# Kernel optimization log

Hardware: AMD Instinct MI355X
Metric: run time of the kernel (lower is better)

The kernel has to match this reference:

```python
import jax, jax.numpy as jnp
import numpy as np

B, S, H, D, R = 16, 2048, 1024, 64, 2048  # batch, seq_len, hidden, inner_dim, num_relations


def setup_inputs() -> dict:
    key = jax.random.key(0)
    k1, k2, k3, k4 = jax.random.split(key, 4)
    last_hidden_state = jax.random.normal(k1, (B, S, H), dtype=jnp.float32)
    W = jax.random.normal(k2, (H, 2 * D), dtype=jnp.float32) * (H ** -0.5)
    b = jnp.zeros((2 * D,), dtype=jnp.float32)
    position_ids = jnp.tile(jnp.arange(S, dtype=jnp.int32), (B, 1))
    relations_idx = jax.random.randint(k3, (B, R, 4), 0, S, dtype=jnp.int32)
    labels_mask = (jax.random.uniform(k4, (B, R)) > 0.1).astype(jnp.float32)
    return {
        'last_hidden_state': last_hidden_state,
        'W': W,
        'b': b,
        'position_ids': position_ids,
        'relations_idx': relations_idx,
        'labels_mask': labels_mask,
    }


def reference(last_hidden_state, W, b, position_ids, relations_idx, labels_mask):
    # linear projection -> split into q/k halves
    outputs = last_hidden_state @ W + b            # [B,S,2D]
    qw, kw = outputs[..., :D], outputs[..., D:]    # each [B,S,D]

    # RoPE (interleaved sin/cos layout matching torch stack+reshape)
    inv_freq = jnp.power(10000.0, -2.0 * jnp.arange(D // 2, dtype=jnp.float32) / D)
    ang = position_ids[..., None].astype(jnp.float32) * inv_freq  # [B,S,D/2]
    sin_pos = jnp.repeat(jnp.sin(ang), 2, axis=-1)  # [B,S,D]
    cos_pos = jnp.repeat(jnp.cos(ang), 2, axis=-1)  # [B,S,D]

    def rotate(x):
        x2 = jnp.stack([-x[..., 1::2], x[..., ::2]], axis=-1).reshape(x.shape)
        return x * cos_pos + x2 * sin_pos

    qw = rotate(qw)
    kw = rotate(kw)

    # gather span endpoints: relations_idx[...,k] -> [B,R], take along seq axis
    def gather(x, idx):
        return jnp.take_along_axis(x, idx[..., None], axis=1)  # [B,R,D]

    sub_qw = jnp.concatenate([gather(qw, relations_idx[:, :, 0]),
                              gather(qw, relations_idx[:, :, 1])], axis=-1)  # [B,R,2D]
    obj_kw = jnp.concatenate([gather(kw, relations_idx[:, :, 2]),
                              gather(kw, relations_idx[:, :, 3])], axis=-1)  # [B,R,2D]

    logits = jnp.sum(sub_qw * obj_kw, axis=-1)     # [B,R]
    logits = logits + (1.0 - labels_mask) * -1e12
    return logits / jnp.sqrt(jnp.float32(D))
```

## Files before the change

### kernel.cpp

```cpp
#include <hip/hip_runtime.h>
#include <hip/hip_bf16.h>
#include <cstdint>

#define B_ 16
#define S_ 2048
#define H_ 1024
#define D_ 64
#define R_ 2048
#define M_ (B_*S_)
#define N_ 128

typedef short short8 __attribute__((ext_vector_type(8)));
typedef float f32x4  __attribute__((ext_vector_type(4)));

__device__ __forceinline__ unsigned short f2bf(float f) {
    unsigned u = __builtin_bit_cast(unsigned, f);
    u += 0x7FFFu + ((u >> 16) & 1u);
    return (unsigned short)(u >> 16);
}

__global__ void build_wt(const float* __restrict__ W, unsigned short* __restrict__ Wt) {
    int o = blockIdx.x * 256 + threadIdx.x;
    int n = o >> 10, k = o & 1023;
    Wt[o] = f2bf(W[k * N_ + n]);
}

__launch_bounds__(256, 2)
__global__ void gemm_rope(const float* __restrict__ A,
                          const unsigned short* __restrict__ Wt,
                          const float* __restrict__ bias,
                          const int* __restrict__ pos_ids,
                          float* __restrict__ qk)
{
    __shared__ unsigned short lw[N_ * 64];

    const int tid  = threadIdx.x;
    const int wave = tid >> 6, lane = tid & 63;
    const int ln15 = lane & 15, quad = lane >> 4;
    const int m    = blockIdx.x * 64 + wave * 16 + ln15;
    const float* arow = A + (size_t)m * H_ + quad * 8;

    f32x4 acc[8];
    #pragma unroll
    for (int j = 0; j < 8; j++) acc[j] = (f32x4)0.f;

    const int wn = tid >> 1, wh = tid & 1;
    const unsigned short* wsrc = Wt + wn * H_ + wh * 32;
    unsigned short* wdst = lw + wn * 64;
    const int wn7 = wn & 7;

    f32x4 a_cur[4], a_nxt[4];
    #pragma unroll
    for (int i = 0; i < 4; i++)
        a_cur[i] = *(const f32x4*)(arow + ((i >> 1) * 32) + ((i & 1) * 4));

    for (int kc = 0; kc < H_; kc += 64) {
        #pragma unroll
        for (int g = 0; g < 4; g++) {
            int gg = wh * 4 + g;
            short8 v = *(const short8*)(wsrc + kc + g * 8);
            *(short8*)(wdst + ((gg ^ wn7) * 8)) = v;
        }
        __syncthreads();

        if (kc + 64 < H_) {
            #pragma unroll
            for (int i = 0; i < 4; i++)
                a_nxt[i] = *(const f32x4*)(arow + (kc + 64) + ((i >> 1) * 32) + ((i & 1) * 4));
        }

        #pragma unroll
        for (int ks = 0; ks < 2; ks++) {
            short8 af;
            #pragma unroll
            for (int i = 0; i < 4; i++) {
                af[i]     = (short)f2bf(a_cur[2 * ks][i]);
                af[i + 4] = (short)f2bf(a_cur[2 * ks + 1][i]);
            }
            const int swz = ((ks * 4 + quad) ^ (ln15 & 7)) * 8;
            #pragma unroll
            for (int j = 0; j < 8; j++) {
                short8 bf = *(const short8*)(lw + (j * 16 + ln15) * 64 + swz);
                acc[j] = __builtin_amdgcn_mfma_f32_16x16x32_bf16(af, bf, acc[j], 0, 0, 0);
            }
        }
        __syncthreads();
        #pragma unroll
        for (int i = 0; i < 4; i++) a_cur[i] = a_nxt[i];
    }

    const int rbase = blockIdx.x * 64 + wave * 16 + quad * 4;
    #pragma unroll
    for (int reg = 0; reg < 4; reg++) {
        const int r = rbase + reg;
        const float pos = (float)pos_ids[r];
        #pragma unroll
        for (int j = 0; j < 8; j++) {
            const int c = j * 16 + ln15;
            float v = acc[j][reg] + bias[c];
            float p = __shfl_xor(v, 1, 64);
            const int fi = (c & 63) >> 1;
            const float ang = pos * exp2f((float)fi * -0.41524101186092029f);
            float s, co;
            sincosf(ang, &s, &co);
            const float outv = (ln15 & 1) ? (v * co + p * s) : (v * co - p * s);
            qk[(size_t)r * N_ + c] = outv;
        }
    }
}

__global__ void gather_dot(const float* __restrict__ qk, const int* __restrict__ rel,
                           const float* __restrict__ mask, float* __restrict__ out)
{
    const int w    = (blockIdx.x * 256 + threadIdx.x) >> 6;
    const int lane = threadIdx.x & 63;
    const int b = w >> 11;
    const int4 id4 = ((const int4*)rel)[w];
    const float* base = qk + (size_t)b * S_ * N_;
    float v = base[(size_t)id4.x * N_ + lane]      * base[(size_t)id4.z * N_ + 64 + lane]
            + base[(size_t)id4.y * N_ + lane]      * base[(size_t)id4.w * N_ + 64 + lane];
    #pragma unroll
    for (int off = 32; off; off >>= 1) v += __shfl_xor(v, off, 64);
    if (lane == 0)
        out[w] = (v + (1.0f - mask[w]) * -1e12f) * 0.125f;
}

extern "C" void kernel_launch(void* const* d_in, const int* in_sizes, int n_in,
                              void* d_out, int out_size, void* d_ws, size_t ws_size,
                              hipStream_t stream) {
    const float* lhs  = (const float*)d_in[0];
    const float* W    = (const float*)d_in[1];
    const float* bias = (const float*)d_in[2];
    const int*   pos  = (const int*)d_in[3];
    const int*   rel  = (const int*)d_in[4];
    const float* mask = (const float*)d_in[5];
    float* out = (float*)d_out;

    unsigned short* Wt = (unsigned short*)d_ws;
    float* qk = (float*)((char*)d_ws + (size_t)N_ * H_ * 2);

    build_wt<<<512, 256, 0, stream>>>(W, Wt);
    gemm_rope<<<512, 256, 0, stream>>>(lhs, Wt, bias, pos, qk);
    gather_dot<<<8192, 256, 0, stream>>>(qk, rel, mask, out);
}
```

Baseline: 228.5 us.

## Double-buffer A and W via direct global-to-LDS loads, store q/k as bf16

Replaces the register-staged A prefetch and per-thread W copy with global_load_lds async loads into double-buffered, XOR-swizzled LDS tiles. The aim is to overlap memory with MFMA and drop one barrier per k-step. The epilogue now uses hardware sin/cos on fractional turns with hoisted bias and frequency values. The q/k intermediate is packed to bf16 pairs, which halves its write and the gather traffic. This costs some accuracy in RoPE and in the stored q/k values, and raises LDS use.

```diff
diff --git a/kernel.cpp b/kernel.cpp
--- a/kernel.cpp
+++ b/kernel.cpp
@@ -9,6 +9,7 @@
 #define R_ 2048
 #define M_ (B_*S_)
 #define N_ 128
+#define NC_ 16
 
 typedef short short8 __attribute__((ext_vector_type(8)));
 typedef float f32x4  __attribute__((ext_vector_type(4)));
@@ -17,6 +18,21 @@
     unsigned u = __builtin_bit_cast(unsigned, f);
     u += 0x7FFFu + ((u >> 16) & 1u);
     return (unsigned short)(u >> 16);
+}
+__device__ __forceinline__ unsigned pk2(float a, float b) {
+    return (unsigned)f2bf(a) | ((unsigned)f2bf(b) << 16);
+}
+__device__ __forceinline__ float bflo(unsigned u) {
+    return __builtin_bit_cast(float, u << 16);
+}
+__device__ __forceinline__ float bfhi(unsigned u) {
+    return __builtin_bit_cast(float, u & 0xFFFF0000u);
+}
+
+typedef const __attribute__((address_space(1))) void gvoid_t;
+typedef __attribute__((address_space(3))) void lvoid_t;
+__device__ __forceinline__ void gload16(const void* g, void* l) {
+    __builtin_amdgcn_global_load_lds((gvoid_t*)g, (lvoid_t*)l, 16, 0, 0);
 }
 
 __global__ void build_wt(const float* __restrict__ W, unsigned short* __restrict__ Wt) {
@@ -30,66 +46,82 @@
                           const unsigned short* __restrict__ Wt,
                           const float* __restrict__ bias,
                           const int* __restrict__ pos_ids,
-                          float* __restrict__ qk)
+                          unsigned* __restrict__ qk)
 {
-    __shared__ unsigned short lw[N_ * 64];
+    __shared__ __align__(16) float          abuf[2][64 * 64];
+    __shared__ __align__(16) unsigned short wbuf[2][N_ * 64];
 
     const int tid  = threadIdx.x;
     const int wave = tid >> 6, lane = tid & 63;
-    const int ln15 = lane & 15, quad = lane >> 4;
-    const int m    = blockIdx.x * 64 + wave * 16 + ln15;
-    const float* arow = A + (size_t)m * H_ + quad * 8;
+    const int ln15 = lane & 15, quad = lane >> 4, key = ln15 & 7;
+    const int m0   = blockIdx.x * 64;
+
+    const float* a_g[4];
+    const unsigned short* w_g[4];
+    int a_lo[4], w_lo[4];
+    #pragma unroll
+    for (int t = 0; t < 4; t++) {
+        const int rl = wave * 16 + t * 4 + (lane >> 4);
+        a_g[t]  = A + (size_t)(m0 + rl) * H_ + (((lane & 15) ^ (rl & 7)) << 2);
+        a_lo[t] = (wave * 16 + t * 4) * 64;
+        const int n = (wave * 4 + t) * 8 + (lane >> 3);
+        w_g[t]  = Wt + (size_t)n * 1024 + (((lane & 7) ^ (n & 7)) << 3);
+        w_lo[t] = (wave * 4 + t) * 8 * 64;
+    }
 
     f32x4 acc[8];
     #pragma unroll
     for (int j = 0; j < 8; j++) acc[j] = (f32x4)0.f;
 
-    const int wn = tid >> 1, wh = tid & 1;
-    const unsigned short* wsrc = Wt + wn * H_ + wh * 32;
-    unsigned short* wdst = lw + wn * 64;
-    const int wn7 = wn & 7;
+    #pragma unroll
+    for (int t = 0; t < 4; t++) {
+        gload16(a_g[t], &abuf[0][a_lo[t]]);
+        gload16(w_g[t], &wbuf[0][w_lo[t]]);
+    }
 
-    f32x4 a_cur[4], a_nxt[4];
-    #pragma unroll
-    for (int i = 0; i < 4; i++)
-        a_cur[i] = *(const f32x4*)(arow + ((i >> 1) * 32) + ((i & 1) * 4));
-
-    for (int kc = 0; kc < H_; kc += 64) {
-        #pragma unroll
-        for (int g = 0; g < 4; g++) {
-            int gg = wh * 4 + g;
-            short8 v = *(const short8*)(wsrc + kc + g * 8);
-            *(short8*)(wdst + ((gg ^ wn7) * 8)) = v;
+    const float* ab_lane_base;
+    for (int kc = 0; kc < NC_; kc++) {
+        __syncthreads();
+        if (kc + 1 < NC_) {
+            const int nb = (kc + 1) & 1;
+            #pragma unroll
+            for (int t = 0; t < 4; t++) {
+                gload16(a_g[t] + (kc + 1) * 64, &abuf[nb][a_lo[t]]);
+                gload16(w_g[t] + (kc + 1) * 64, &wbuf[nb][w_lo[t]]);
+            }
         }
-        __syncthreads();
-
-        if (kc + 64 < H_) {
-            #pragma unroll
-            for (int i = 0; i < 4; i++)
-                a_nxt[i] = *(const f32x4*)(arow + (kc + 64) + ((i >> 1) * 32) + ((i & 1) * 4));
-        }
-
+        const int cb = kc & 1;
+        ab_lane_base = &abuf[cb][(wave * 16 + ln15) * 64];
         #pragma unroll
         for (int ks = 0; ks < 2; ks++) {
-            short8 af;
-            #pragma unroll
-            for (int i = 0; i < 4; i++) {
-                af[i]     = (short)f2bf(a_cur[2 * ks][i]);
-                af[i + 4] = (short)f2bf(a_cur[2 * ks + 1][i]);
-            }
-            const int swz = ((ks * 4 + quad) ^ (ln15 & 7)) * 8;
+            const int g0 = ks * 8 + quad * 2;
+            f32x4 r0 = *(const f32x4*)(ab_lane_base + ((g0 ^ key) << 2));
+            f32x4 r1 = *(const f32x4*)(ab_lane_base + (((g0 + 1) ^ key) << 2));
+            int4 ai;
+            ai.x = (int)pk2(r0[0], r0[1]);
+            ai.y = (int)pk2(r0[2], r0[3]);
+            ai.z = (int)pk2(r1[0], r1[1]);
+            ai.w = (int)pk2(r1[2], r1[3]);
+            const short8 af = __builtin_bit_cast(short8, ai);
+            const int p = ((ks * 4 + quad) ^ key) << 3;
             #pragma unroll
             for (int j = 0; j < 8; j++) {
-                short8 bf = *(const short8*)(lw + (j * 16 + ln15) * 64 + swz);
+                const short8 bf = *(const short8*)(&wbuf[cb][(j * 16 + ln15) * 64 + p]);
                 acc[j] = __builtin_amdgcn_mfma_f32_16x16x32_bf16(af, bf, acc[j], 0, 0, 0);
             }
         }
-        __syncthreads();
-        #pragma unroll
-        for (int i = 0; i < 4; i++) a_cur[i] = a_nxt[i];
     }
 
-    const int rbase = blockIdx.x * 64 + wave * 16 + quad * 4;
+    const int rbase = m0 + wave * 16 + quad * 4;
+    float bv[8], invr[4];
+    #pragma unroll
+    for (int j = 0; j < 8; j++) bv[j] = bias[j * 16 + ln15];
+    #pragma unroll
+    for (int jj = 0; jj < 4; jj++) {
+        const float fi = (float)((jj * 16 + ln15) >> 1);
+        invr[jj] = exp2f(fi * -0.41524101186092029f) * 0.15915494309189535f;
+    }
+    const bool odd = (ln15 & 1);
     #pragma unroll
     for (int reg = 0; reg < 4; reg++) {
         const int r = rbase + reg;
@@ -97,28 +129,33 @@
         #pragma unroll
         for (int j = 0; j < 8; j++) {
             const int c = j * 16 + ln15;
-            float v = acc[j][reg] + bias[c];
+            float v = acc[j][reg] + bv[j];
             float p = __shfl_xor(v, 1, 64);
-            const int fi = (c & 63) >> 1;
-            const float ang = pos * exp2f((float)fi * -0.41524101186092029f);
-            float s, co;
-            sincosf(ang, &s, &co);
-            const float outv = (ln15 & 1) ? (v * co + p * s) : (v * co - p * s);
-            qk[(size_t)r * N_ + c] = outv;
+            float fr = __builtin_amdgcn_fractf(pos * invr[j & 3]);
+            float s  = __builtin_amdgcn_sinf(fr);
+            float co = __builtin_amdgcn_cosf(fr);
+            float outv = odd ? fmaf(v, co, p * s) : fmaf(v, co, -p * s);
+            float po = __shfl_xor(outv, 1, 64);
+            if (!odd)
+                qk[(size_t)r * 64 + (c >> 1)] = pk2(outv, po);
         }
     }
 }
 
-__global__ void gather_dot(const float* __restrict__ qk, const int* __restrict__ rel,
+__global__ void gather_dot(const unsigned* __restrict__ qk, const int* __restrict__ rel,
                            const float* __restrict__ mask, float* __restrict__ out)
 {
     const int w    = (blockIdx.x * 256 + threadIdx.x) >> 6;
     const int lane = threadIdx.x & 63;
-    const int b = w >> 11;
+    const int b    = w >> 11;
     const int4 id4 = ((const int4*)rel)[w];
-    const float* base = qk + (size_t)b * S_ * N_;
-    float v = base[(size_t)id4.x * N_ + lane]      * base[(size_t)id4.z * N_ + 64 + lane]
-            + base[(size_t)id4.y * N_ + lane]      * base[(size_t)id4.w * N_ + 64 + lane];
+    const unsigned* base = qk + (size_t)b * S_ * 64;
+    const int rq  = (lane < 32) ? id4.x : id4.y;
+    const int rk  = (lane < 32) ? id4.z : id4.w;
+    const int col = lane & 31;
+    const unsigned uq = base[(size_t)rq * 64 + col];
+    const unsigned uk = base[(size_t)rk * 64 + 32 + col];
+    float v = bflo(uq) * bflo(uk) + bfhi(uq) * bfhi(uk);
     #pragma unroll
     for (int off = 32; off; off >>= 1) v += __shfl_xor(v, off, 64);
     if (lane == 0)
@@ -137,7 +174,7 @@
     float* out = (float*)d_out;
 
     unsigned short* Wt = (unsigned short*)d_ws;
-    float* qk = (float*)((char*)d_ws + (size_t)N_ * H_ * 2);
+    unsigned* qk = (unsigned*)((char*)d_ws + (size_t)N_ * H_ * 2);
 
     build_wt<<<512, 256, 0, stream>>>(W, Wt);
     gemm_rope<<<512, 256, 0, stream>>>(lhs, Wt, bias, pos, qk);
```

New measurement: 220.6 us. 3.5% less time.
